# Kernel tuning notes

Measured on AMD Instinct MI355X. Metric: run time of the kernel, lower is better.

The kernel has to match this reference:

```python
import jax, jax.numpy as jnp
import numpy as np

N_NODES = 50000
N_EDGES = 800000
IN_FEAT = 128
N_HEADS = 4
OUT_FEAT = 16
NEG_SLOPE = 0.2


def setup_inputs() -> dict:
    key = jax.random.key(0)
    k1, k2, k3, k4, k5 = jax.random.split(key, 5)
    x = jax.random.normal(k1, (N_NODES, IN_FEAT), dtype=jnp.float32)
    src = jax.random.randint(k2, (N_EDGES,), 0, N_NODES)
    dst = jax.random.randint(k3, (N_EDGES,), 0, N_NODES)
    edge_index = jnp.stack([src, dst]).astype(jnp.int64)
    # xavier-uniform-like init for params
    limW = np.sqrt(6.0 / (IN_FEAT + N_HEADS * OUT_FEAT))
    W = jax.random.uniform(k4, (IN_FEAT, N_HEADS * OUT_FEAT), minval=-limW, maxval=limW, dtype=jnp.float32)
    lima = np.sqrt(6.0 / (N_HEADS + 2 * OUT_FEAT))
    a = jax.random.uniform(k5, (1, N_HEADS, 2 * OUT_FEAT), minval=-lima, maxval=lima, dtype=jnp.float32)
    return {"x": x, "edge_index": edge_index, "W": W, "a": a}


def reference(x, edge_index, W, a):
    N = x.shape[0]
    H = a.shape[1]
    F = a.shape[2] // 2
    src, dst = edge_index[0], edge_index[1]
    # node projection: [N, H, F]
    h = (x @ W).reshape(N, H, F)
    # split attention vector: sum(a * cat(h_src, h_dst)) = a_src.h_src + a_dst.h_dst
    a_src = a[0, :, :F]  # [H, F]
    a_dst = a[0, :, F:]  # [H, F]
    e_src = jnp.einsum('nhf,hf->nh', h, a_src)  # [N, H]
    e_dst = jnp.einsum('nhf,hf->nh', h, a_dst)  # [N, H]
    edge_e = jax.nn.leaky_relu(e_src[src] + e_dst[dst], NEG_SLOPE)  # [E, H]
    # softmax over heads (dim=1 in the source)
    alpha = jax.nn.softmax(edge_e, axis=1)  # [E, H]
    # dropout is identity in eval mode
    msg = alpha[:, :, None] * h[src]  # [E, H, F]
    out = jax.ops.segment_sum(msg, dst, num_segments=N)  # [N, H, F]
    # concat=True
    return out.reshape(N, H * F)
```

## Files before the change

kernel.cpp:

```cpp
#include <hip/hip_runtime.h>
#include <hip/hip_bf16.h>

#define IN_FEAT 128
#define N_HEADS 4
#define OUT_FEAT 16
#define HF 64
#define NEG_SLOPE 0.2f

#define BSHIFT 7
#define BNODES 128
#define NBUCK_MAX 512

typedef __hip_bfloat16 bf16;
typedef __attribute__((ext_vector_type(8))) short short8;
typedef __attribute__((ext_vector_type(4))) float f32x4;

__device__ inline unsigned short f2b(float f) {
  bf16 b = __float2bfloat16(f);
  return *(unsigned short*)&b;
}
__device__ inline float b2f(unsigned short u) {
  return __uint_as_float((unsigned)u << 16);
}

__global__ __launch_bounds__(256) void k_gemm(
    const float* __restrict__ x, const float* __restrict__ W,
    const float* __restrict__ a, unsigned short* __restrict__ h16,
    float* __restrict__ e_src, float* __restrict__ e_dst,
    const int* __restrict__ dst, int* __restrict__ bh,
    int n_nodes, int n_edges, int nbuck, int chunkE, int gb) {
  __shared__ unsigned short xs[64][136];
  __shared__ unsigned short wt[64][136];
  __shared__ unsigned short sh[64][68];
  __shared__ int bhist[NBUCK_MAX];
  const int t = threadIdx.x;
  const int nb = blockIdx.x * 64;
  const int lane = t & 63;
  const int w = t >> 6;

  for (int i = t; i < NBUCK_MAX; i += 256) bhist[i] = 0;

  const float4* x4 = (const float4*)x;
  for (int i = t; i < 64 * 32; i += 256) {
    int n = i >> 5, k4 = i & 31;
    int gn = nb + n;
    float4 v = (gn < n_nodes) ? x4[(size_t)gn * 32 + k4]
                              : make_float4(0.f, 0.f, 0.f, 0.f);
    ushort4 u;
    u.x = f2b(v.x); u.y = f2b(v.y); u.z = f2b(v.z); u.w = f2b(v.w);
    *(ushort4*)&xs[n][k4 * 4] = u;
  }
  for (int i = t; i < IN_FEAT * HF; i += 256) {
    int k = i >> 6, c = i & 63;
    wt[c][k] = f2b(W[i]);
  }
  __syncthreads();

  const int m = lane & 15;
  const int q = lane >> 4;
  f32x4 acc[4];
#pragma unroll
  for (int nt = 0; nt < 4; ++nt) acc[nt] = (f32x4){0.f, 0.f, 0.f, 0.f};

#pragma unroll
  for (int kc = 0; kc < 4; ++kc) {
    short8 af = *(const short8*)&xs[w * 16 + m][kc * 32 + q * 8];
#pragma unroll
    for (int nt = 0; nt < 4; ++nt) {
      short8 bfr = *(const short8*)&wt[nt * 16 + m][kc * 32 + q * 8];
      acc[nt] = __builtin_amdgcn_mfma_f32_16x16x32_bf16(af, bfr, acc[nt], 0, 0, 0);
    }
  }

#pragma unroll
  for (int nt = 0; nt < 4; ++nt)
#pragma unroll
    for (int r = 0; r < 4; ++r)
      sh[w * 16 + q * 4 + r][nt * 16 + m] = f2b(acc[nt][r]);
  __syncthreads();

  {
    int n = t >> 2, hd = t & 3;
    int gn = nb + n;
    if (gn < n_nodes) {
      float es = 0.f, ed = 0.f;
#pragma unroll
      for (int f = 0; f < OUT_FEAT; ++f) {
        float hv = b2f(sh[n][hd * 16 + f]);
        es = fmaf(hv, a[hd * 2 * OUT_FEAT + f], es);
        ed = fmaf(hv, a[hd * 2 * OUT_FEAT + OUT_FEAT + f], ed);
      }
      e_src[gn * N_HEADS + hd] = es;
      e_dst[gn * N_HEADS + hd] = ed;
    }
  }

  for (int i = t; i < 64 * 16; i += 256) {
    int n = i >> 4, c4 = (i & 15) * 4;
    int gn = nb + n;
    if (gn < n_nodes) {
      ushort4 v;
      v.x = sh[n][c4 + 0]; v.y = sh[n][c4 + 1];
      v.z = sh[n][c4 + 2]; v.w = sh[n][c4 + 3];
      *(ushort4*)(h16 + (size_t)gn * HF + c4) = v;
    }
  }

  {
    int ebeg = blockIdx.x * chunkE;
    int eend = min(ebeg + chunkE, n_edges);
    for (int e = ebeg + t; e < eend; e += 256)
      atomicAdd(&bhist[dst[e] >> BSHIFT], 1);
    __syncthreads();
    for (int k = t; k < nbuck; k += 256)
      bh[(size_t)k * gb + blockIdx.x] = bhist[k];
  }
}

__global__ __launch_bounds__(1024) void k_scanA(
    const int* __restrict__ bh, int* __restrict__ sbase, int* __restrict__ tot,
    int gb) {
  __shared__ int s[1024];
  int t = threadIdx.x, k = blockIdx.x;
  int v = (t < gb) ? bh[(size_t)k * gb + t] : 0;
  s[t] = v;
  __syncthreads();
  for (int off = 1; off < 1024; off <<= 1) {
    int u = (t >= off) ? s[t - off] : 0;
    __syncthreads();
    s[t] += u;
    __syncthreads();
  }
  if (t < gb) sbase[(size_t)k * gb + t] = s[t] - v;
  if (t == 1023) tot[k] = s[t];
}

__global__ __launch_bounds__(512) void k_scanB(
    const int* __restrict__ tot, int* __restrict__ bucket_base,
    int* __restrict__ offsets, int nbuck, int n_edges, int n_nodes) {
  __shared__ int s[512];
  int t = threadIdx.x;
  int v = (t < nbuck) ? tot[t] : 0;
  s[t] = v;
  __syncthreads();
  for (int off = 1; off < 512; off <<= 1) {
    int u = (t >= off) ? s[t - off] : 0;
    __syncthreads();
    s[t] += u;
    __syncthreads();
  }
  if (t < nbuck) bucket_base[t] = s[t] - v;
  if (t == 0) {
    bucket_base[nbuck] = n_edges;
    offsets[n_nodes] = n_edges;
  }
}

__global__ __launch_bounds__(256) void k_part(
    const int* __restrict__ src, const int* __restrict__ dst,
    const float* __restrict__ e_src, const float* __restrict__ e_dst,
    const int* __restrict__ bucket_base, const int* __restrict__ sbase,
    uint4* __restrict__ recs, int nbuck, int chunkE, int n_edges, int gb) {
  __shared__ int cur[NBUCK_MAX];
  int t = threadIdx.x;
  for (int k = t; k < nbuck; k += 256)
    cur[k] = bucket_base[k] + sbase[(size_t)k * gb + blockIdx.x];
  __syncthreads();
  int beg = blockIdx.x * chunkE;
  int end = min(beg + chunkE, n_edges);
  for (int e = beg + t; e < end; e += 256) {
    int s = src[e], d = dst[e];
    float4 es = ((const float4*)e_src)[s];
    float4 ed = ((const float4*)e_dst)[d];
    float v0 = es.x + ed.x, v1 = es.y + ed.y, v2 = es.z + ed.z, v3 = es.w + ed.w;
    v0 = (v0 > 0.f) ? v0 : NEG_SLOPE * v0;
    v1 = (v1 > 0.f) ? v1 : NEG_SLOPE * v1;
    v2 = (v2 > 0.f) ? v2 : NEG_SLOPE * v2;
    v3 = (v3 > 0.f) ? v3 : NEG_SLOPE * v3;
    float m = fmaxf(fmaxf(v0, v1), fmaxf(v2, v3));
    float e0 = __expf(v0 - m), e1 = __expf(v1 - m);
    float e2 = __expf(v2 - m), e3 = __expf(v3 - m);
    float inv = 1.f / (e0 + e1 + e2 + e3);
    unsigned lo = (unsigned)f2b(e0 * inv) | ((unsigned)f2b(e1 * inv) << 16);
    unsigned hi = (unsigned)f2b(e2 * inv) | ((unsigned)f2b(e3 * inv) << 16);
    int pos = atomicAdd(&cur[d >> BSHIFT], 1);
    recs[pos] = make_uint4((unsigned)s, (unsigned)(d & (BNODES - 1)), lo, hi);
  }
}

__global__ __launch_bounds__(512) void k_sort(
    const uint4* __restrict__ recs, const int* __restrict__ bucket_base,
    uint4* __restrict__ sorted16, int* __restrict__ offsets,
    int nbuck, int n_nodes) {
  __shared__ int hist[BNODES];
  __shared__ int cur[BNODES];
  int t = threadIdx.x, k = blockIdx.x;
  int beg = bucket_base[k];
  int n = bucket_base[k + 1] - beg;
  if (t < BNODES) hist[t] = 0;
  __syncthreads();
  {
    int j = t;
    for (; j + 1536 < n; j += 2048) {
      unsigned y0 = recs[beg + j].y;
      unsigned y1 = recs[beg + j + 512].y;
      unsigned y2 = recs[beg + j + 1024].y;
      unsigned y3 = recs[beg + j + 1536].y;
      atomicAdd(&hist[y0], 1);
      atomicAdd(&hist[y1], 1);
      atomicAdd(&hist[y2], 1);
      atomicAdd(&hist[y3], 1);
    }
    for (; j < n; j += 512) atomicAdd(&hist[recs[beg + j].y], 1);
  }
  __syncthreads();
  int v = (t < BNODES) ? hist[t] : 0;
  for (int off = 1; off < BNODES; off <<= 1) {
    int u = (t < BNODES && t >= off) ? hist[t - off] : 0;
    __syncthreads();
    if (t < BNODES) hist[t] += u;
    __syncthreads();
  }
  if (t < BNODES) {
    int pos = beg + hist[t] - v;
    cur[t] = pos;
    int node = (k << BSHIFT) + t;
    if (node < n_nodes) offsets[node] = pos;
  }
  __syncthreads();
  {
    int j = t;
    for (; j + 1536 < n; j += 2048) {
      uint4 r0 = recs[beg + j];
      uint4 r1 = recs[beg + j + 512];
      uint4 r2 = recs[beg + j + 1024];
      uint4 r3 = recs[beg + j + 1536];
      int p0 = atomicAdd(&cur[r0.y], 1);
      int p1 = atomicAdd(&cur[r1.y], 1);
      int p2 = atomicAdd(&cur[r2.y], 1);
      int p3 = atomicAdd(&cur[r3.y], 1);
      sorted16[p0] = make_uint4(r0.x, 0u, r0.z, r0.w);
      sorted16[p1] = make_uint4(r1.x, 0u, r1.z, r1.w);
      sorted16[p2] = make_uint4(r2.x, 0u, r2.z, r2.w);
      sorted16[p3] = make_uint4(r3.x, 0u, r3.z, r3.w);
    }
    for (; j < n; j += 512) {
      uint4 r = recs[beg + j];
      int p = atomicAdd(&cur[r.y], 1);
      sorted16[p] = make_uint4(r.x, 0u, r.z, r.w);
    }
  }
}

__global__ __launch_bounds__(256) void k_gather(
    const uint4* __restrict__ sorted16, const int* __restrict__ offsets,
    const unsigned short* __restrict__ h16, float* __restrict__ out,
    int n_nodes) {
  int gid = blockIdx.x * 256 + threadIdx.x;
  int d = gid >> 6;
  if (d >= n_nodes) return;
  int lane = threadIdx.x & 63;
  int half = lane >> 5;
  int c2 = lane & 31;
  unsigned sel = (unsigned)(c2 >> 3);
  unsigned shamt = (sel & 1u) * 16u;
  int beg = offsets[d];
  int end = offsets[d + 1];
  const unsigned* h32 = (const unsigned*)h16;
  float a0 = 0.f, a1 = 0.f;
  for (int j = beg; j < end; j += 16) {
    uint4 r[8];
#pragma unroll
    for (int k = 0; k < 8; ++k) {
      int idx = j + 2 * k + half;
      int cidx = (idx < end) ? idx : (end - 1);
      r[k] = sorted16[cidx];
    }
    unsigned hv[8];
#pragma unroll
    for (int k = 0; k < 8; ++k)
      hv[k] = h32[(size_t)r[k].x * (HF / 2) + c2];
#pragma unroll
    for (int k = 0; k < 8; ++k) {
      int idx = j + 2 * k + half;
      unsigned wd = (sel & 2u) ? r[k].w : r[k].z;
      float al = __uint_as_float(((wd >> shamt) & 0xffffu) << 16);
      al = (idx < end) ? al : 0.f;
      a0 = fmaf(al, b2f((unsigned short)(hv[k] & 0xffffu)), a0);
      a1 = fmaf(al, b2f((unsigned short)(hv[k] >> 16)), a1);
    }
  }
  a0 += __shfl_xor(a0, 32);
  a1 += __shfl_xor(a1, 32);
  if (half == 0) {
    float2 v = make_float2(a0, a1);
    *(float2*)(out + (size_t)d * HF + 2 * c2) = v;
  }
}

extern "C" void kernel_launch(void* const* d_in, const int* in_sizes, int n_in,
                              void* d_out, int out_size, void* d_ws, size_t ws_size,
                              hipStream_t stream) {
  const float* x = (const float*)d_in[0];
  const int* ei = (const int*)d_in[1];
  const float* W = (const float*)d_in[2];
  const float* a = (const float*)d_in[3];
  float* out = (float*)d_out;

  const int n_nodes = in_sizes[0] / IN_FEAT;
  const int n_edges = in_sizes[1] / 2;
  const int* src = ei;
  const int* dst = ei + n_edges;

  const int nbuck = (n_nodes + BNODES - 1) >> BSHIFT;
  const int gb = (n_nodes + 63) / 64;
  const int chunkE = (n_edges + gb - 1) / gb;

  char* ws = (char*)d_ws;
  size_t off = 0;
  uint4* recs = (uint4*)(ws + off);        off += (size_t)n_edges * 16;
  uint4* sorted16 = (uint4*)(ws + off);    off += (size_t)n_edges * 16;
  unsigned short* h16 = (unsigned short*)(ws + off); off += (size_t)n_nodes * HF * 2;
  float* e_src = (float*)(ws + off);       off += (size_t)n_nodes * N_HEADS * 4;
  float* e_dst = (float*)(ws + off);       off += (size_t)n_nodes * N_HEADS * 4;
  int* bh = (int*)(ws + off);              off += (size_t)NBUCK_MAX * gb * 4;
  int* sbase = (int*)(ws + off);           off += (size_t)NBUCK_MAX * gb * 4;
  int* tot = (int*)(ws + off);             off += (size_t)NBUCK_MAX * 4;
  int* bucket_base = (int*)(ws + off);     off += (size_t)(NBUCK_MAX + 1) * 4;
  int* offsets = (int*)(ws + off);         off += ((size_t)n_nodes + 16) * 4;

  k_gemm<<<gb, 256, 0, stream>>>(x, W, a, h16, e_src, e_dst, dst, bh,
                                 n_nodes, n_edges, nbuck, chunkE, gb);
  k_scanA<<<nbuck, 1024, 0, stream>>>(bh, sbase, tot, gb);
  k_scanB<<<1, 512, 0, stream>>>(tot, bucket_base, offsets, nbuck, n_edges, n_nodes);
  k_part<<<gb, 256, 0, stream>>>(src, dst, e_src, e_dst, bucket_base, sbase,
                                 recs, nbuck, chunkE, n_edges, gb);
  k_sort<<<nbuck, 512, 0, stream>>>(recs, bucket_base, sorted16, offsets, nbuck, n_nodes);
  k_gather<<<((size_t)n_nodes * 64 + 255) / 256, 256, 0, stream>>>(
      sorted16, offsets, h16, out, n_nodes);
}
```

Baseline: 161.1 us.

## Fuse scan kernels via last-block pattern and add XCD-aware block swizzle

Merges the second scan kernel into the first: each scanA block bumps a global counter, and the last block to finish scans the per-bucket totals, which removes one kernel launch. Separately, the partition, sort and gather kernels remap blockIdx so that consecutive logical blocks land on the same XCD of the MI355X, aiming to improve L2 locality. The cost is threadfence and atomic overhead plus a counter that k_gemm must reset on every launch.

```diff
diff --git a/kernel.cpp b/kernel.cpp
--- a/kernel.cpp
+++ b/kernel.cpp
@@ -10,6 +10,7 @@
 #define BSHIFT 7
 #define BNODES 128
 #define NBUCK_MAX 512
+#define NXCD 8
 
 typedef __hip_bfloat16 bf16;
 typedef __attribute__((ext_vector_type(8))) short short8;
@@ -21,13 +22,18 @@
 }
 __device__ inline float b2f(unsigned short u) {
   return __uint_as_float((unsigned)u << 16);
+}
+__device__ inline int xcd_swz(int b, int n) {
+  int q = n >> 3, r = n & 7;
+  int x = b & 7, i = b >> 3;
+  return (x < r) ? x * (q + 1) + i : r * (q + 1) + (x - r) * q + i;
 }
 
 __global__ __launch_bounds__(256) void k_gemm(
     const float* __restrict__ x, const float* __restrict__ W,
     const float* __restrict__ a, unsigned short* __restrict__ h16,
     float* __restrict__ e_src, float* __restrict__ e_dst,
-    const int* __restrict__ dst, int* __restrict__ bh,
+    const int* __restrict__ dst, int* __restrict__ bh, int* __restrict__ done,
     int n_nodes, int n_edges, int nbuck, int chunkE, int gb) {
   __shared__ unsigned short xs[64][136];
   __shared__ unsigned short wt[64][136];
@@ -38,6 +44,7 @@
   const int lane = t & 63;
   const int w = t >> 6;
 
+  if (blockIdx.x == 0 && t == 0) *done = 0;
   for (int i = t; i < NBUCK_MAX; i += 256) bhist[i] = 0;
 
   const float4* x4 = (const float4*)x;
@@ -119,8 +126,10 @@
 
 __global__ __launch_bounds__(1024) void k_scanA(
     const int* __restrict__ bh, int* __restrict__ sbase, int* __restrict__ tot,
-    int gb) {
+    int* __restrict__ bucket_base, int* __restrict__ offsets,
+    int* __restrict__ done, int gb, int nbuck, int n_edges, int n_nodes) {
   __shared__ int s[1024];
+  __shared__ int amLast;
   int t = threadIdx.x, k = blockIdx.x;
   int v = (t < gb) ? bh[(size_t)k * gb + t] : 0;
   s[t] = v;
@@ -132,24 +141,23 @@
     __syncthreads();
   }
   if (t < gb) sbase[(size_t)k * gb + t] = s[t] - v;
-  if (t == 1023) tot[k] = s[t];
-}
-
-__global__ __launch_bounds__(512) void k_scanB(
-    const int* __restrict__ tot, int* __restrict__ bucket_base,
-    int* __restrict__ offsets, int nbuck, int n_edges, int n_nodes) {
-  __shared__ int s[512];
-  int t = threadIdx.x;
-  int v = (t < nbuck) ? tot[t] : 0;
-  s[t] = v;
-  __syncthreads();
-  for (int off = 1; off < 512; off <<= 1) {
+  if (t == 1023) tot[k] = s[1023];
+  __threadfence();
+  __syncthreads();
+  if (t == 0) amLast = (atomicAdd(done, 1) == nbuck - 1) ? 1 : 0;
+  __syncthreads();
+  if (!amLast) return;
+  __threadfence();
+  int w = (t < nbuck) ? tot[t] : 0;
+  s[t] = w;
+  __syncthreads();
+  for (int off = 1; off < 1024; off <<= 1) {
     int u = (t >= off) ? s[t - off] : 0;
     __syncthreads();
     s[t] += u;
     __syncthreads();
   }
-  if (t < nbuck) bucket_base[t] = s[t] - v;
+  if (t < nbuck) bucket_base[t] = s[t] - w;
   if (t == 0) {
     bucket_base[nbuck] = n_edges;
     offsets[n_nodes] = n_edges;
@@ -163,10 +171,11 @@
     uint4* __restrict__ recs, int nbuck, int chunkE, int n_edges, int gb) {
   __shared__ int cur[NBUCK_MAX];
   int t = threadIdx.x;
+  int chunk = xcd_swz(blockIdx.x, gb);
   for (int k = t; k < nbuck; k += 256)
-    cur[k] = bucket_base[k] + sbase[(size_t)k * gb + blockIdx.x];
-  __syncthreads();
-  int beg = blockIdx.x * chunkE;
+    cur[k] = bucket_base[k] + sbase[(size_t)k * gb + chunk];
+  __syncthreads();
+  int beg = chunk * chunkE;
   int end = min(beg + chunkE, n_edges);
   for (int e = beg + t; e < end; e += 256) {
     int s = src[e], d = dst[e];
@@ -194,7 +203,8 @@
     int nbuck, int n_nodes) {
   __shared__ int hist[BNODES];
   __shared__ int cur[BNODES];
-  int t = threadIdx.x, k = blockIdx.x;
+  int t = threadIdx.x;
+  int k = xcd_swz(blockIdx.x, nbuck);
   int beg = bucket_base[k];
   int n = bucket_base[k + 1] - beg;
   if (t < BNODES) hist[t] = 0;
@@ -255,8 +265,9 @@
 __global__ __launch_bounds__(256) void k_gather(
     const uint4* __restrict__ sorted16, const int* __restrict__ offsets,
     const unsigned short* __restrict__ h16, float* __restrict__ out,
-    int n_nodes) {
-  int gid = blockIdx.x * 256 + threadIdx.x;
+    int n_nodes, int ngb) {
+  int g = xcd_swz(blockIdx.x, ngb);
+  int gid = g * 256 + threadIdx.x;
   int d = gid >> 6;
   if (d >= n_nodes) return;
   int lane = threadIdx.x & 63;
@@ -315,6 +326,7 @@
   const int nbuck = (n_nodes + BNODES - 1) >> BSHIFT;
   const int gb = (n_nodes + 63) / 64;
   const int chunkE = (n_edges + gb - 1) / gb;
+  const int ngb = (n_nodes * 64 + 255) / 256;
 
   char* ws = (char*)d_ws;
   size_t off = 0;
@@ -328,14 +340,14 @@
   int* tot = (int*)(ws + off);             off += (size_t)NBUCK_MAX * 4;
   int* bucket_base = (int*)(ws + off);     off += (size_t)(NBUCK_MAX + 1) * 4;
   int* offsets = (int*)(ws + off);         off += ((size_t)n_nodes + 16) * 4;
-
-  k_gemm<<<gb, 256, 0, stream>>>(x, W, a, h16, e_src, e_dst, dst, bh,
+  int* done = (int*)(ws + off);            off += 64;
+
+  k_gemm<<<gb, 256, 0, stream>>>(x, W, a, h16, e_src, e_dst, dst, bh, done,
                                  n_nodes, n_edges, nbuck, chunkE, gb);
-  k_scanA<<<nbuck, 1024, 0, stream>>>(bh, sbase, tot, gb);
-  k_scanB<<<1, 512, 0, stream>>>(tot, bucket_base, offsets, nbuck, n_edges, n_nodes);
+  k_scanA<<<nbuck, 1024, 0, stream>>>(bh, sbase, tot, bucket_base, offsets,
+                                      done, gb, nbuck, n_edges, n_nodes);
   k_part<<<gb, 256, 0, stream>>>(src, dst, e_src, e_dst, bucket_base, sbase,
                                  recs, nbuck, chunkE, n_edges, gb);
   k_sort<<<nbuck, 512, 0, stream>>>(recs, bucket_base, sorted16, offsets, nbuck, n_nodes);
-  k_gather<<<((size_t)n_nodes * 64 + 255) / 256, 256, 0, stream>>>(
-      sorted16, offsets, h16, out, n_nodes);
-}
+  k_gather<<<ngb, 256, 0, stream>>>(sorted16, offsets, h16, out, n_nodes, ngb);
+}
```

Measured after the change: 259.5 us. 61.1% more time.
